# Performance work log

Hardware: AMD Instinct MI355X
Metric: run time of the kernel (lower is better)

## Reference

```python
import jax, jax.numpy as jnp
import numpy as np

DIM = 768      # model dim
NHEAD = 12     # heads
HD = DIM // NHEAD
SCALE = HD ** -0.5
B = 8          # batch
SPEC = 4       # spec_frames
T = 8          # num_frames // 2
AP = 196       # audio_patch (kv tokens per spec frame)
VP = 196       # vmae spatial patches (q tokens per frame)


def setup_inputs() -> dict:
    key = jax.random.key(0)
    ks = jax.random.split(key, 10)
    f = lambda k, sh: jax.random.normal(k, sh, dtype=jnp.float32)
    return {
        "s_x": f(ks[0], (AP, B * SPEC, DIM)),
        "t_x": f(ks[1], (1 + VP, B * T, DIM)),
        "clip_space_pos": SCALE * f(ks[2], (AP, DIM)),
        "clip_temporal_pos": SCALE * f(ks[3], (SPEC, DIM)),
        "vmae_space_pos": SCALE * f(ks[4], (VP, DIM)),
        "vmae_temporal_pos": SCALE * f(ks[5], (T, DIM)),
        "Wq": 0.02 * f(ks[6], (DIM, DIM)),
        "q_bias": jnp.zeros((DIM,), jnp.float32),
        "Wkv": 0.02 * f(ks[7], (2 * DIM, DIM)),
        "kv_bias": jnp.zeros((2 * DIM,), jnp.float32),
        "Wproj": 0.02 * f(ks[8], (DIM, DIM)),
        "proj_bias": jnp.zeros((DIM,), jnp.float32),
    }


def reference(s_x, t_x, clip_space_pos, clip_temporal_pos, vmae_space_pos,
              vmae_temporal_pos, Wq, q_bias, Wkv, kv_bias, Wproj, proj_bias):
    # attn_all_frame=True path of CrossAttentionS2T.s2t_cross_attn
    t_cls, t_pat = t_x[:1], t_x[1:]

    # s_x: (n, b*st, d) -> b st n d, + space pos; -> b n st d, + temporal pos; -> b (n st) d
    s = s_x.reshape(AP, B, SPEC, DIM).transpose(1, 2, 0, 3) + clip_space_pos
    s = s.transpose(0, 2, 1, 3) + clip_temporal_pos
    s = s.reshape(B, AP * SPEC, DIM)

    # t_x_pat: (n, b*t, d) -> b t n d, + space pos; -> b n t d, + temporal pos; -> b (n t) d
    q_in = t_pat.reshape(VP, B, T, DIM).transpose(1, 2, 0, 3) + vmae_space_pos
    q_in = q_in.transpose(0, 2, 1, 3) + vmae_temporal_pos
    q_in = q_in.reshape(B, VP * T, DIM)

    # Q projection: [B, Nq, D] -> [B, H, Nq, hd], pre-scaled
    q = (q_in @ Wq.T + q_bias).reshape(B, VP * T, NHEAD, HD).transpose(0, 2, 1, 3) * SCALE
    # KV projection: [B, Nk, 2D] -> split (e h d) order
    kv = (s @ Wkv.T + kv_bias).reshape(B, AP * SPEC, 2, NHEAD, HD)
    k = kv[:, :, 0].transpose(0, 2, 1, 3)  # [B, H, Nk, hd]
    v = kv[:, :, 1].transpose(0, 2, 1, 3)

    attn = jax.nn.softmax(jnp.einsum('bhqd,bhkd->bhqk', q, k), axis=-1)
    o = jnp.einsum('bhqk,bhkd->bhqd', attn, v)
    o = o.transpose(0, 2, 1, 3).reshape(B, VP * T, DIM)
    o = o @ Wproj.T + proj_bias

    # 'b (n t) d -> n (b t) d'
    o = o.reshape(B, VP, T, DIM).transpose(1, 0, 2, 3).reshape(VP, B * T, DIM)
    return jnp.concatenate([t_cls, o], axis=0)
```

## Files before the change

kernel.cpp:

```cpp
#include <hip/hip_runtime.h>
#include <stdint.h>

#define DIM 768
#define NHEAD 12
#define HD 64
#define B_ 8
#define SPEC 4
#define T_ 8
#define AP 196
#define VP 196
#define MQ (VP*T_)
#define NKV (AP*SPEC)
#define NG2 50
#define QSCALE 0.1803368801111618f

typedef short bf16x8 __attribute__((ext_vector_type(8)));
typedef short bf16x4 __attribute__((ext_vector_type(4)));
typedef float f32x4 __attribute__((ext_vector_type(4)));

__device__ __forceinline__ ushort f2bf(float f) {
    union { float f; unsigned u; } v; v.f = f;
    unsigned u = v.u;
    return (ushort)((u + 0x7fffu + ((u >> 16) & 1u)) >> 16);
}

__device__ __forceinline__ float fexp2(float x) {
    float r;
    asm("v_exp_f32 %0, %1" : "=v"(r) : "v"(x));
    return r;
}

__device__ __forceinline__ unsigned pk2(float a, float b) {
    union { float f; unsigned u; } ua, ub; ua.f = a; ub.f = b;
    return (ub.u & 0xFFFF0000u) | (ua.u >> 16);
}

typedef const __attribute__((address_space(1))) void GV;
typedef __attribute__((address_space(3))) void LV;
__device__ __forceinline__ void gload16(const void* g, void* l) {
    __builtin_amdgcn_global_load_lds((GV*)g, (LV*)l, 16, 0, 0);
}


__global__ void prep_all_k(const float* __restrict__ t_x,
                           const float* __restrict__ vsp,
                           const float* __restrict__ vtp,
                           const float* __restrict__ s_x,
                           const float* __restrict__ csp,
                           const float* __restrict__ ctp,
                           const float* __restrict__ Wq,
                           const float* __restrict__ Wkv,
                           const float* __restrict__ Wpj,
                           ushort* __restrict__ qin,
                           ushort* __restrict__ sb,
                           ushort* __restrict__ wqb,
                           ushort* __restrict__ wkvb,
                           ushort* __restrict__ wpjb,
                           float* __restrict__ out) {
    int bid = blockIdx.x;
    if (bid < 9408) {
        int i = bid * 256 + threadIdx.x;
        int d4 = i % (DIM / 4);
        int rest = i / (DIM / 4);
        int m = rest % MQ;
        int b = rest / MQ;
        int vp = m >> 3, t = m & 7;
        const float4 a  = *(const float4*)(t_x + ((size_t)(1 + vp) * (B_ * T_) + b * T_ + t) * DIM + d4 * 4);
        const float4 p1 = *(const float4*)(vsp + (size_t)vp * DIM + d4 * 4);
        const float4 p2 = *(const float4*)(vtp + (size_t)t * DIM + d4 * 4);
        ushort4 r;
        r.x = f2bf(a.x + p1.x + p2.x);
        r.y = f2bf(a.y + p1.y + p2.y);
        r.z = f2bf(a.z + p1.z + p2.z);
        r.w = f2bf(a.w + p1.w + p2.w);
        *(ushort4*)(qin + ((size_t)(b * MQ + m)) * DIM + d4 * 4) = r;
    } else if (bid < 14112) {
        int i = (bid - 9408) * 256 + threadIdx.x;
        int d4 = i % (DIM / 4);
        int rest = i / (DIM / 4);
        int n = rest % NKV;
        int b = rest / NKV;
        int ap = n >> 2, spec = n & 3;
        const float4 a  = *(const float4*)(s_x + ((size_t)ap * (B_ * SPEC) + b * SPEC + spec) * DIM + d4 * 4);
        const float4 p1 = *(const float4*)(csp + (size_t)ap * DIM + d4 * 4);
        const float4 p2 = *(const float4*)(ctp + (size_t)spec * DIM + d4 * 4);
        ushort4 r;
        r.x = f2bf(a.x + p1.x + p2.x);
        r.y = f2bf(a.y + p1.y + p2.y);
        r.z = f2bf(a.z + p1.z + p2.z);
        r.w = f2bf(a.w + p1.w + p2.w);
        *(ushort4*)(sb + ((size_t)(b * NKV + n)) * DIM + d4 * 4) = r;
    } else if (bid < 16416) {
        const float* src; ushort* dst; int i;
        if (bid < 14688)      { src = Wq;  dst = wqb;  i = (bid - 14112) * 256 + threadIdx.x; }
        else if (bid < 15840) { src = Wkv; dst = wkvb; i = (bid - 14688) * 256 + threadIdx.x; }
        else                  { src = Wpj; dst = wpjb; i = (bid - 15840) * 256 + threadIdx.x; }
        float4 v = *(const float4*)(src + (size_t)i * 4);
        ushort4 r;
        r.x = f2bf(v.x); r.y = f2bf(v.y); r.z = f2bf(v.z); r.w = f2bf(v.w);
        *(ushort4*)(dst + (size_t)i * 4) = r;
    } else {
        int i = (bid - 16416) * 256 + threadIdx.x;
        *(float4*)(out + (size_t)i * 4) = *(const float4*)(t_x + (size_t)i * 4);
    }
}


template <int MODE>
__device__ __forceinline__ void gemm_body(ushort* As, ushort* Bs,
                                          const ushort* __restrict__ A,
                                          const ushort* __restrict__ Bw,
                                          const float* __restrict__ bias,
                                          ushort* __restrict__ out_a,
                                          ushort* __restrict__ out_b,
                                          float* __restrict__ out_f,
                                          int m0, int n0) {
    const int tid = threadIdx.x;
    const int lane = tid & 63, wid = tid >> 6;
    const int wm = wid >> 1, wn = wid & 1;
    const int lr = lane & 15, hi = lane >> 4;

    const int srow = wid * 32 + (lane >> 2);
    const int scolb = (lane & 3) * 16;
    const char* gA = (const char*)A + ((size_t)(m0 + srow) * DIM) * 2 + scolb;
    const char* gB = (const char*)Bw + ((size_t)(n0 + srow) * DIM) * 2 + scolb;
    const size_t radv = (size_t)16 * DIM * 2;
    char* lA = (char*)As + wid * 2048;
    char* lB = (char*)Bs + wid * 2048;

    f32x4 acc[4][4] = {};

    for (int k0 = 0; k0 < DIM; k0 += 32) {
        size_t ko = (size_t)k0 * 2;
        gload16(gA + ko,        lA);
        gload16(gA + ko + radv, lA + 1024);
        gload16(gB + ko,        lB);
        gload16(gB + ko + radv, lB + 1024);
        __syncthreads();
        bf16x8 af[4], bfr[4];
#pragma unroll
        for (int x = 0; x < 4; ++x) {
            af[x]  = *(const bf16x8*)&As[(wm * 64 + x * 16 + lr) * 32 + hi * 8];
            bfr[x] = *(const bf16x8*)&Bs[(wn * 64 + x * 16 + lr) * 32 + hi * 8];
        }
#pragma unroll
        for (int mi = 0; mi < 4; ++mi)
#pragma unroll
            for (int ni = 0; ni < 4; ++ni)
                acc[mi][ni] = __builtin_amdgcn_mfma_f32_16x16x32_bf16(af[mi], bfr[ni], acc[mi][ni], 0, 0, 0);
        __syncthreads();
    }

#pragma unroll
    for (int mi = 0; mi < 4; ++mi) {
#pragma unroll
        for (int ni = 0; ni < 4; ++ni) {
            int gn = n0 + wn * 64 + ni * 16 + lr;
            float bv = bias[gn];
            if (MODE == 1 && gn >= DIM) {
                int o2 = gn - DIM;
                int hh = o2 >> 6, d = o2 & 63;
                int gm0 = m0 + wm * 64 + mi * 16 + hi * 4;
                int b = gm0 / NKV, n = gm0 % NKV;
                int bh = b * NHEAD + hh;
                int g2 = n >> 4, c = n & 15;
                ushort4 pk;
                pk.x = f2bf(acc[mi][ni][0] + bv);
                pk.y = f2bf(acc[mi][ni][1] + bv);
                pk.z = f2bf(acc[mi][ni][2] + bv);
                pk.w = f2bf(acc[mi][ni][3] + bv);
                *(ushort4*)&out_b[(((size_t)(bh * NG2 + g2)) * 64 + d) * 16 + c] = pk;
                continue;
            }
#pragma unroll
            for (int r = 0; r < 4; ++r) {
                int gm = m0 + wm * 64 + mi * 16 + hi * 4 + r;
                float val = acc[mi][ni][r] + bv;
                if (MODE == 0) {
                    int b = gm / MQ, m = gm % MQ;
                    int hh = gn >> 6, d = gn & 63;
                    out_a[(((size_t)(b * NHEAD + hh)) * MQ + m) * HD + d] = f2bf(val * QSCALE);
                } else if (MODE == 1) {
                    int b = gm / NKV, n = gm % NKV;
                    int hh = gn >> 6, d = gn & 63;
                    out_a[(((size_t)(b * NHEAD + hh)) * NKV + n) * HD + d] = f2bf(val);
                } else {
                    int b = gm / MQ, m = gm % MQ;
                    int vp = m >> 3, tt = m & 7;
                    out_f[((size_t)(1 + vp) * (B_ * T_) + b * T_ + tt) * DIM + gn] = val;
                }
            }
        }
    }
}

__global__ __launch_bounds__(256) void gemm_qkv_k(const ushort* __restrict__ qin,
                                                  const ushort* __restrict__ sbuf,
                                                  const ushort* __restrict__ wqb,
                                                  const ushort* __restrict__ wkvb,
                                                  const float* __restrict__ qb,
                                                  const float* __restrict__ kvb,
                                                  ushort* __restrict__ qs,
                                                  ushort* __restrict__ kb,
                                                  ushort* __restrict__ vtb) {
    __shared__ __align__(16) ushort As[128 * 32];
    __shared__ __align__(16) ushort Bs[128 * 32];
    int d = blockIdx.x;
    int w = (d & 7) * 147 + (d >> 3);
    if (w < 588) {
        int by = w / 6, bx = w % 6;
        gemm_body<0>(As, Bs, qin, wqb, qb, qs, nullptr, nullptr, by * 128, bx * 128);
    } else {
        int w2 = w - 588;
        int by = w2 / 12, bx = w2 % 12;
        gemm_body<1>(As, Bs, sbuf, wkvb, kvb, kb, vtb, nullptr, by * 128, bx * 128);
    }
}

__global__ __launch_bounds__(256) void gemm_proj_k(const ushort* __restrict__ ob,
                                                   const ushort* __restrict__ wpjb,
                                                   const float* __restrict__ pjb,
                                                   float* __restrict__ out) {
    __shared__ __align__(16) ushort As[128 * 32];
    __shared__ __align__(16) ushort Bs[128 * 32];
    int d = blockIdx.x;
    int xcd = d & 7;
    int w = (xcd < 4 ? xcd * 74 : 296 + (xcd - 4) * 73) + (d >> 3);
    int by = w / 6, bx = w % 6;
    gemm_body<2>(As, Bs, ob, wpjb, pjb, nullptr, nullptr, out, by * 128, bx * 128);
}


template <int NT>
__device__ __forceinline__ void attn_wave(const ushort* __restrict__ q,
                                          const ushort* __restrict__ kp,
                                          const ushort* __restrict__ vtp,
                                          ushort* __restrict__ obuf,
                                          int bh, int b, int h, int m0, int lane) {
    const int lr = lane & 15, hi = lane >> 4;

    bf16x8 qa0[NT], qa1[NT];
#pragma unroll
    for (int t = 0; t < NT; ++t) {
        const ushort* qp = q + ((size_t)bh * MQ + m0 + t * 16 + lr) * HD;
        qa0[t] = *(const bf16x8*)(qp + hi * 8);
        qa1[t] = *(const bf16x8*)(qp + 32 + hi * 8);
    }

    f32x4 oacc[NT][4] = {};
    float lsum[NT] = {};

    bf16x8 kA[4], kB[4], kC[4];
    bf16x4 vAa[4], vAb[4], vBa[4], vBb[4];
    {
        const ushort* ka = kp + (size_t)lr * HD + hi * 8;
        kA[0] = *(const bf16x8*)ka;
        kA[1] = *(const bf16x8*)(ka + 32);
        kA[2] = *(const bf16x8*)(ka + 16 * HD);
        kA[3] = *(const bf16x8*)(ka + 16 * HD + 32);
        const ushort* kb1 = ka + 32 * HD;
        kB[0] = *(const bf16x8*)kb1;
        kB[1] = *(const bf16x8*)(kb1 + 32);
        kB[2] = *(const bf16x8*)(kb1 + 16 * HD);
        kB[3] = *(const bf16x8*)(kb1 + 16 * HD + 32);
        const ushort* vp = vtp + (lr * 16 + hi * 4);
#pragma unroll
        for (int db = 0; db < 4; ++db) {
            vAa[db] = *(const bf16x4*)(vp + db * 256);
            vAb[db] = *(const bf16x4*)(vp + db * 256 + 1024);
        }
    }

    auto gbody = [&](bf16x8* kc, bf16x8* kpre, bf16x4* vca, bf16x4* vcb,
                     bf16x4* vna, bf16x4* vnb, int g) {
        const int nk = g * 32 + 64;
        const int nv = g * 32 + 32;
        {
            const ushort* ka = kp + (size_t)(nk + lr) * HD + hi * 8;
            kpre[0] = *(const bf16x8*)ka;
            kpre[1] = *(const bf16x8*)(ka + 32);
            kpre[2] = *(const bf16x8*)(ka + 16 * HD);
            kpre[3] = *(const bf16x8*)(ka + 16 * HD + 32);
        }
        {
            const ushort* vp = vtp + (size_t)(nv >> 4) * 1024 + (lr * 16 + hi * 4);
#pragma unroll
            for (int db = 0; db < 4; ++db) {
                vna[db] = *(const bf16x4*)(vp + db * 256);
                vnb[db] = *(const bf16x4*)(vp + db * 256 + 1024);
            }
        }
        __builtin_amdgcn_s_setprio(1);
#pragma unroll
        for (int t = 0; t < NT; ++t) {
            f32x4 sA = {}, sB = {};
            sA = __builtin_amdgcn_mfma_f32_16x16x32_bf16(kc[0], qa0[t], sA, 0, 0, 0);
            sA = __builtin_amdgcn_mfma_f32_16x16x32_bf16(kc[1], qa1[t], sA, 0, 0, 0);
            sB = __builtin_amdgcn_mfma_f32_16x16x32_bf16(kc[2], qa0[t], sB, 0, 0, 0);
            sB = __builtin_amdgcn_mfma_f32_16x16x32_bf16(kc[3], qa1[t], sB, 0, 0, 0);
            float eA0 = fexp2(sA[0]), eA1 = fexp2(sA[1]), eA2 = fexp2(sA[2]), eA3 = fexp2(sA[3]);
            float eB0 = fexp2(sB[0]), eB1 = fexp2(sB[1]), eB2 = fexp2(sB[2]), eB3 = fexp2(sB[3]);
            lsum[t] += ((eA0 + eA1) + (eA2 + eA3)) + ((eB0 + eB1) + (eB2 + eB3));
            union { uint4 w; bf16x8 v; } pk;
            pk.w.x = pk2(eA0, eA1);
            pk.w.y = pk2(eA2, eA3);
            pk.w.z = pk2(eB0, eB1);
            pk.w.w = pk2(eB2, eB3);
#pragma unroll
            for (int db = 0; db < 4; ++db) {
                union { struct { bf16x4 lo, hi_; } s; bf16x8 v; } vf;
                vf.s.lo = vca[db]; vf.s.hi_ = vcb[db];
                oacc[t][db] = __builtin_amdgcn_mfma_f32_16x16x32_bf16(pk.v, vf.v, oacc[t][db], 0, 0, 0);
            }
        }
        __builtin_amdgcn_s_setprio(0);
    };

    for (int gp = 0; gp < 24; gp += 6) {
        gbody(kA, kC, vAa, vAb, vBa, vBb, gp);
        gbody(kB, kA, vBa, vBb, vAa, vAb, gp + 1);
        gbody(kC, kB, vAa, vAb, vBa, vBb, gp + 2);
        gbody(kA, kC, vBa, vBb, vAa, vAb, gp + 3);
        gbody(kB, kA, vAa, vAb, vBa, vBb, gp + 4);
        gbody(kC, kB, vBa, vBb, vAa, vAb, gp + 5);
    }

    {
#pragma unroll
        for (int t = 0; t < NT; ++t) {
            f32x4 sA = {};
            sA = __builtin_amdgcn_mfma_f32_16x16x32_bf16(kA[0], qa0[t], sA, 0, 0, 0);
            sA = __builtin_amdgcn_mfma_f32_16x16x32_bf16(kA[1], qa1[t], sA, 0, 0, 0);
            float eA0 = fexp2(sA[0]), eA1 = fexp2(sA[1]), eA2 = fexp2(sA[2]), eA3 = fexp2(sA[3]);
            lsum[t] += (eA0 + eA1) + (eA2 + eA3);
            union { uint4 w; bf16x8 v; } pk;
            pk.w.x = pk2(eA0, eA1);
            pk.w.y = pk2(eA2, eA3);
            pk.w.z = 0;
            pk.w.w = 0;
#pragma unroll
            for (int db = 0; db < 4; ++db) {
                union { struct { bf16x4 lo, hi_; } s; bf16x8 v; } vf;
                vf.s.lo = vAa[db]; vf.s.hi_ = vAa[db];
                oacc[t][db] = __builtin_amdgcn_mfma_f32_16x16x32_bf16(pk.v, vf.v, oacc[t][db], 0, 0, 0);
            }
        }
    }

#pragma unroll
    for (int t = 0; t < NT; ++t) {
        float sum = lsum[t];
        sum += __shfl_xor(sum, 16);
        sum += __shfl_xor(sum, 32);
        float inv = 1.0f / sum;
#pragma unroll
        for (int r = 0; r < 4; ++r) {
            float invr = __shfl(inv, hi * 4 + r);
            int m = m0 + t * 16 + hi * 4 + r;
            ushort* op = obuf + ((size_t)b * MQ + m) * DIM + h * HD;
#pragma unroll
            for (int db = 0; db < 4; ++db)
                op[db * 16 + lr] = f2bf(oacc[t][db][r] * invr);
        }
    }
}

__global__ __launch_bounds__(128) void attn_k(const ushort* __restrict__ q,
                                              const ushort* __restrict__ kbuf,
                                              const ushort* __restrict__ vt,
                                              ushort* __restrict__ obuf) {
    const int lane = threadIdx.x & 63, wid = threadIdx.x >> 6;
    const int bid = blockIdx.x;
    const int bh = bid % 96;
    const int mb = bid / 96;
    const int b = bh / NHEAD, h = bh % NHEAD;
    const ushort* kp  = kbuf + (size_t)bh * NKV * HD;
    const ushort* vtp = vt + (size_t)bh * NG2 * 1024;
    const int mbase = mb * 112;
    if (wid == 0)
        attn_wave<4>(q, kp, vtp, obuf, bh, b, h, mbase, lane);
    else
        attn_wave<3>(q, kp, vtp, obuf, bh, b, h, mbase + 64, lane);
}


extern "C" void kernel_launch(void* const* d_in, const int* in_sizes, int n_in,
                              void* d_out, int out_size, void* d_ws, size_t ws_size,
                              hipStream_t stream) {
    const float* s_x  = (const float*)d_in[0];
    const float* t_x  = (const float*)d_in[1];
    const float* csp  = (const float*)d_in[2];
    const float* ctp  = (const float*)d_in[3];
    const float* vsp  = (const float*)d_in[4];
    const float* vtp  = (const float*)d_in[5];
    const float* Wq   = (const float*)d_in[6];
    const float* qb   = (const float*)d_in[7];
    const float* Wkv  = (const float*)d_in[8];
    const float* kvb  = (const float*)d_in[9];
    const float* Wpj  = (const float*)d_in[10];
    const float* pjb  = (const float*)d_in[11];
    float* out = (float*)d_out;

    ushort* w = (ushort*)d_ws;
    ushort* qin  = w; w += (size_t)B_ * MQ * DIM;
    ushort* sb   = w; w += (size_t)B_ * NKV * DIM;
    ushort* wqb  = w; w += (size_t)DIM * DIM;
    ushort* wkvb = w; w += (size_t)2 * DIM * DIM;
    ushort* wpjb = w; w += (size_t)DIM * DIM;
    ushort* qs   = w; w += (size_t)B_ * NHEAD * MQ * HD;
    ushort* kb   = w; w += (size_t)B_ * NHEAD * NKV * HD;
    ushort* vtb  = w; w += (size_t)B_ * NHEAD * NG2 * 1024;
    ushort* ob   = w; w += (size_t)B_ * MQ * DIM;

    prep_all_k<<<16464, 256, 0, stream>>>(t_x, vsp, vtp, s_x, csp, ctp,
                                          Wq, Wkv, Wpj,
                                          qin, sb, wqb, wkvb, wpjb, out);

    gemm_qkv_k<<<1176, 256, 0, stream>>>(qin, sb, wqb, wkvb, qb, kvb, qs, kb, vtb);

    attn_k<<<1344, 128, 0, stream>>>(qs, kb, vtb, ob);

    gemm_proj_k<<<588, 256, 0, stream>>>(ob, wpjb, pjb, out);
}
```

Measured before the change: 152.1 us.

## Repack V into 32-key blocks for 16-byte loads and deepen prefetch

The QKV GEMM epilogue now writes V transposed into 32-key groups, with the column positions permuted so each lane's eight bf16 values for the PV MFMA sit contiguously. The attention wave can then load V with single 16-byte loads instead of pairs of 8-byte loads and feed them to the MFMA without repacking. The K/V software pipeline is also deepened to four K buffers (prefetching three groups ahead) and three V buffers (two ahead), with the loop unrolled by 12. This raises register pressure and changes the workspace layout. The tail group relies on zero-padded entries in the new layout.

```diff
diff --git a/kernel.cpp b/kernel.cpp
--- a/kernel.cpp
+++ b/kernel.cpp
@@ -11,7 +11,7 @@
 #define VP 196
 #define MQ (VP*T_)
 #define NKV (AP*SPEC)
-#define NG2 50
+#define NG32 26
 #define QSCALE 0.1803368801111618f
 
 typedef short bf16x8 __attribute__((ext_vector_type(8)));
@@ -163,13 +163,14 @@
                 int gm0 = m0 + wm * 64 + mi * 16 + hi * 4;
                 int b = gm0 / NKV, n = gm0 % NKV;
                 int bh = b * NHEAD + hh;
-                int g2 = n >> 4, c = n & 15;
+                int g32 = n >> 5, nl = n & 31;
+                int cpos = ((nl >> 2) & 3) * 8 + (nl >> 4) * 4;
                 ushort4 pk;
                 pk.x = f2bf(acc[mi][ni][0] + bv);
                 pk.y = f2bf(acc[mi][ni][1] + bv);
                 pk.z = f2bf(acc[mi][ni][2] + bv);
                 pk.w = f2bf(acc[mi][ni][3] + bv);
-                *(ushort4*)&out_b[(((size_t)(bh * NG2 + g2)) * 64 + d) * 16 + c] = pk;
+                *(ushort4*)&out_b[(((size_t)(bh * NG32 + g32)) * 64 + d) * 32 + cpos] = pk;
                 continue;
             }
 #pragma unroll
@@ -250,46 +251,29 @@
     f32x4 oacc[NT][4] = {};
     float lsum[NT] = {};
 
-    bf16x8 kA[4], kB[4], kC[4];
-    bf16x4 vAa[4], vAb[4], vBa[4], vBb[4];
-    {
-        const ushort* ka = kp + (size_t)lr * HD + hi * 8;
-        kA[0] = *(const bf16x8*)ka;
-        kA[1] = *(const bf16x8*)(ka + 32);
-        kA[2] = *(const bf16x8*)(ka + 16 * HD);
-        kA[3] = *(const bf16x8*)(ka + 16 * HD + 32);
-        const ushort* kb1 = ka + 32 * HD;
-        kB[0] = *(const bf16x8*)kb1;
-        kB[1] = *(const bf16x8*)(kb1 + 32);
-        kB[2] = *(const bf16x8*)(kb1 + 16 * HD);
-        kB[3] = *(const bf16x8*)(kb1 + 16 * HD + 32);
-        const ushort* vp = vtp + (lr * 16 + hi * 4);
-#pragma unroll
-        for (int db = 0; db < 4; ++db) {
-            vAa[db] = *(const bf16x4*)(vp + db * 256);
-            vAb[db] = *(const bf16x4*)(vp + db * 256 + 1024);
-        }
-    }
-
-    auto gbody = [&](bf16x8* kc, bf16x8* kpre, bf16x4* vca, bf16x4* vcb,
-                     bf16x4* vna, bf16x4* vnb, int g) {
-        const int nk = g * 32 + 64;
-        const int nv = g * 32 + 32;
-        {
-            const ushort* ka = kp + (size_t)(nk + lr) * HD + hi * 8;
-            kpre[0] = *(const bf16x8*)ka;
-            kpre[1] = *(const bf16x8*)(ka + 32);
-            kpre[2] = *(const bf16x8*)(ka + 16 * HD);
-            kpre[3] = *(const bf16x8*)(ka + 16 * HD + 32);
-        }
-        {
-            const ushort* vp = vtp + (size_t)(nv >> 4) * 1024 + (lr * 16 + hi * 4);
-#pragma unroll
-            for (int db = 0; db < 4; ++db) {
-                vna[db] = *(const bf16x4*)(vp + db * 256);
-                vnb[db] = *(const bf16x4*)(vp + db * 256 + 1024);
-            }
-        }
+    bf16x8 kA[4], kB[4], kC[4], kD[4];
+    bf16x8 vA[4], vB[4], vC[4];
+
+    auto kload = [&](bf16x8* dst, int g) {
+        const ushort* ka = kp + (size_t)(g * 32 + lr) * HD + hi * 8;
+        dst[0] = *(const bf16x8*)ka;
+        dst[1] = *(const bf16x8*)(ka + 32);
+        dst[2] = *(const bf16x8*)(ka + 16 * HD);
+        dst[3] = *(const bf16x8*)(ka + 16 * HD + 32);
+    };
+    auto vload = [&](bf16x8* dst, int g) {
+        const ushort* vp = vtp + (size_t)g * 2048 + (size_t)lr * 32 + hi * 8;
+#pragma unroll
+        for (int db = 0; db < 4; ++db)
+            dst[db] = *(const bf16x8*)(vp + db * 512);
+    };
+
+    kload(kA, 0); kload(kB, 1); kload(kC, 2);
+    vload(vA, 0); vload(vB, 1);
+
+    auto gbody = [&](bf16x8* kc, bf16x8* kpre, bf16x8* vc, bf16x8* vpre, int g) {
+        kload(kpre, g + 3);
+        vload(vpre, g + 2);
         __builtin_amdgcn_s_setprio(1);
 #pragma unroll
         for (int t = 0; t < NT; ++t) {
@@ -307,22 +291,25 @@
             pk.w.z = pk2(eB0, eB1);
             pk.w.w = pk2(eB2, eB3);
 #pragma unroll
-            for (int db = 0; db < 4; ++db) {
-                union { struct { bf16x4 lo, hi_; } s; bf16x8 v; } vf;
-                vf.s.lo = vca[db]; vf.s.hi_ = vcb[db];
-                oacc[t][db] = __builtin_amdgcn_mfma_f32_16x16x32_bf16(pk.v, vf.v, oacc[t][db], 0, 0, 0);
-            }
+            for (int db = 0; db < 4; ++db)
+                oacc[t][db] = __builtin_amdgcn_mfma_f32_16x16x32_bf16(pk.v, vc[db], oacc[t][db], 0, 0, 0);
         }
         __builtin_amdgcn_s_setprio(0);
     };
 
-    for (int gp = 0; gp < 24; gp += 6) {
-        gbody(kA, kC, vAa, vAb, vBa, vBb, gp);
-        gbody(kB, kA, vBa, vBb, vAa, vAb, gp + 1);
-        gbody(kC, kB, vAa, vAb, vBa, vBb, gp + 2);
-        gbody(kA, kC, vBa, vBb, vAa, vAb, gp + 3);
-        gbody(kB, kA, vAa, vAb, vBa, vBb, gp + 4);
-        gbody(kC, kB, vBa, vBb, vAa, vAb, gp + 5);
+    for (int gp = 0; gp < 24; gp += 12) {
+        gbody(kA, kD, vA, vC, gp);
+        gbody(kB, kA, vB, vA, gp + 1);
+        gbody(kC, kB, vC, vB, gp + 2);
+        gbody(kD, kC, vA, vC, gp + 3);
+        gbody(kA, kD, vB, vA, gp + 4);
+        gbody(kB, kA, vC, vB, gp + 5);
+        gbody(kC, kB, vA, vC, gp + 6);
+        gbody(kD, kC, vB, vA, gp + 7);
+        gbody(kA, kD, vC, vB, gp + 8);
+        gbody(kB, kA, vA, vC, gp + 9);
+        gbody(kC, kB, vB, vA, gp + 10);
+        gbody(kD, kC, vC, vB, gp + 11);
     }
 
     {
@@ -339,11 +326,8 @@
             pk.w.z = 0;
             pk.w.w = 0;
 #pragma unroll
-            for (int db = 0; db < 4; ++db) {
-                union { struct { bf16x4 lo, hi_; } s; bf16x8 v; } vf;
-                vf.s.lo = vAa[db]; vf.s.hi_ = vAa[db];
-                oacc[t][db] = __builtin_amdgcn_mfma_f32_16x16x32_bf16(pk.v, vf.v, oacc[t][db], 0, 0, 0);
-            }
+            for (int db = 0; db < 4; ++db)
+                oacc[t][db] = __builtin_amdgcn_mfma_f32_16x16x32_bf16(pk.v, vA[db], oacc[t][db], 0, 0, 0);
         }
     }
 
@@ -375,7 +359,7 @@
     const int mb = bid / 96;
     const int b = bh / NHEAD, h = bh % NHEAD;
     const ushort* kp  = kbuf + (size_t)bh * NKV * HD;
-    const ushort* vtp = vt + (size_t)bh * NG2 * 1024;
+    const ushort* vtp = vt + (size_t)bh * NG32 * 2048;
     const int mbase = mb * 112;
     if (wid == 0)
         attn_wave<4>(q, kp, vtp, obuf, bh, b, h, mbase, lane);
@@ -409,7 +393,7 @@
     ushort* wpjb = w; w += (size_t)DIM * DIM;
     ushort* qs   = w; w += (size_t)B_ * NHEAD * MQ * HD;
     ushort* kb   = w; w += (size_t)B_ * NHEAD * NKV * HD;
-    ushort* vtb  = w; w += (size_t)B_ * NHEAD * NG2 * 1024;
+    ushort* vtb  = w; w += (size_t)B_ * NHEAD * NG32 * 2048;
     ushort* ob   = w; w += (size_t)B_ * MQ * DIM;
 
     prep_all_k<<<16464, 256, 0, stream>>>(t_x, vsp, vtp, s_x, csp, ctp,
```

After: 156.9 us. 3.2% more time.
